# Kernel optimization log

Hardware: AMD Instinct MI355X
Metric: run time of the kernel (lower is better)

Reference implementation:

```python
import jax, jax.numpy as jnp
import numpy as np

B, M, FIN = 16, 49152, 16
F1, K = 32, 5
NNZ = 8 * M  # ~8 neighbors per vertex on a HEALPix sphere mesh


def setup_inputs() -> dict:
    key = jax.random.key(0)
    kx, kr, kc, kv, kw, kb = jax.random.split(key, 6)
    x = jax.random.normal(kx, (B, M, FIN), dtype=jnp.float32)
    rows = jax.random.randint(kr, (NNZ,), 0, M, dtype=jnp.int32)
    cols = jax.random.randint(kc, (NNZ,), 0, M, dtype=jnp.int32)
    # small values keep the order-K Chebyshev recurrence numerically tame
    vals = jax.random.normal(kv, (NNZ,), dtype=jnp.float32) * 0.1
    stddev = 1.0 / np.sqrt(FIN * (K + 0.5) / 2.0)
    kernel = jax.random.normal(kw, (FIN * K, F1), dtype=jnp.float32) * stddev
    bias = jax.random.uniform(kb, (1, 1, F1), dtype=jnp.float32) * 0.05
    return {"x": x, "rows": rows, "cols": cols, "vals": vals,
            "kernel": kernel, "bias": bias}


def reference(x, rows, cols, vals, kernel, bias):
    # x: [B, M, Fin]; sparse Laplacian L in COO (rows, cols, vals), shape [M, M]
    b, m, fin = x.shape
    k = kernel.shape[0] // fin

    def spmm(X):  # L @ X for X: [M, Fin*B]
        return jax.ops.segment_sum(vals[:, None] * X[cols], rows, num_segments=m)

    # x0: [M, Fin*B] exactly as the TF transpose/reshape does
    x0 = jnp.transpose(x, (1, 2, 0)).reshape(m, fin * b)
    xs = [x0]
    if k > 1:
        x1 = spmm(x0)
        xs.append(x1)
    for _ in range(2, k):
        x2 = 2.0 * spmm(x1) - x0
        xs.append(x2)
        x0, x1 = x1, x2
    # [K, M, Fin, B] -> [B, M, Fin, K] -> [B*M, Fin*K]
    xk = jnp.stack(xs, axis=0).reshape(k, m, fin, b)
    xk = jnp.transpose(xk, (3, 1, 2, 0)).reshape(b * m, fin * k)
    out = (xk @ kernel).reshape(b, m, -1)  # [B, M, F1]
    return out + bias
```

## Files before the change

### kernel.cpp

```cpp
#include <hip/hip_runtime.h>


constexpr int M   = 49152;
constexpr int B   = 16;
constexpr int FIN = 16;
constexpr int F1  = 32;
constexpr int K   = 5;
constexpr int XBS = M * FIN;
constexpr size_t SLICEB   = (size_t)M * 64;
constexpr size_t BUFBYTES = (size_t)M * 512;
constexpr int NBLK_M = M / 256;
constexpr int NHB = 64 * NBLK_M;

typedef short s16x8 __attribute__((ext_vector_type(8)));
typedef float f32x4 __attribute__((ext_vector_type(4)));
typedef unsigned int u32;
typedef unsigned long long u64;

#define DEVFN __device__ __forceinline__

DEVFN float lo2f(u32 d) {
  union { u32 u; float f; } v; v.u = d << 16; return v.f;
}
DEVFN float hi2f(u32 d) {
  union { u32 u; float f; } v; v.u = d & 0xffff0000u; return v.f;
}
DEVFN unsigned short f2bf(float f) {
  union { float f; u32 u; } v;
  v.f = f;
  u32 r = (v.u + 0x7FFFu + ((v.u >> 16) & 1u)) >> 16;
  return (unsigned short)r;
}


__global__ __launch_bounds__(256) void transform_x(const float* __restrict__ x,
                                                   char* __restrict__ x0b) {
  int lane = threadIdx.x & 63, wave = threadIdx.x >> 6;
  int mchunk = blockIdx.x >> 2, bquad = blockIdx.x & 3;
  int b = bquad * 4 + wave;
  int m = mchunk * 16 + (lane >> 2);
  int f = (lane & 3) * 4;
  float4 v = *(const float4*)(x + (size_t)b * XBS + (size_t)m * FIN + f);
  ushort4 r = make_ushort4(f2bf(v.x), f2bf(v.y), f2bf(v.z), f2bf(v.w));
  *(ushort4*)(x0b + (size_t)(b >> 1) * SLICEB + (size_t)m * 64 +
              (size_t)(b & 1) * 32 + (size_t)(lane & 3) * 8) = r;
}


__global__ __launch_bounds__(256) void hist_kernel(const int* __restrict__ rows,
                                                   int* __restrict__ counts, int nnz) {
  int i = blockIdx.x * 256 + threadIdx.x;
  if (i < nnz) atomicAdd(&counts[rows[i]], 1);
}

__global__ __launch_bounds__(256) void pad_counts(const int* __restrict__ counts,
                                                  int* __restrict__ c8) {
  int m = blockIdx.x * 256 + threadIdx.x;
  c8[m] = (counts[m] + 8) & ~7;
}

DEVFN int wave_incl_scan(int v, int lane) {
#pragma unroll
  for (int off = 1; off < 64; off <<= 1) {
    int t = __shfl_up(v, off);
    if (lane >= off) v += t;
  }
  return v;
}

__global__ __launch_bounds__(1024) void scan_blocks(const int* __restrict__ src,
                                                    int* __restrict__ dst,
                                                    int* __restrict__ partials) {
  __shared__ int wsum[16];
  int tid = threadIdx.x, lane = tid & 63, w = tid >> 6;
  int i = blockIdx.x * 1024 + tid;
  int s = wave_incl_scan(src[i], lane);
  if (lane == 63) wsum[w] = s;
  __syncthreads();
  if (tid < 16) {
    int t = wsum[tid];
#pragma unroll
    for (int off = 1; off < 16; off <<= 1) {
      int u = __shfl_up(t, off);
      if (tid >= off) t += u;
    }
    wsum[tid] = t;
  }
  __syncthreads();
  int base = (w > 0) ? wsum[w - 1] : 0;
  s += base;
  dst[i + 1] = s;
  if (tid == 1023) partials[blockIdx.x] = s;
}

__global__ void scan_partials_kernel(int* __restrict__ partials,
                                     int* __restrict__ dst, int nblk) {
  int lane = threadIdx.x;
  int v = (lane < nblk) ? partials[lane] : 0;
  v = wave_incl_scan(v, lane);
  if (lane < nblk) partials[lane] = v;
  if (lane == 0) dst[0] = 0;
}

__global__ __launch_bounds__(1024) void scan_add_kernel(int* __restrict__ dst,
                                                        const int* __restrict__ partials) {
  if (blockIdx.x == 0) return;
  int i = blockIdx.x * 1024 + threadIdx.x;
  dst[i + 1] += partials[blockIdx.x - 1];
}

__global__ __launch_bounds__(256) void scatter_kernel(const int* __restrict__ rows,
                                                      const int* __restrict__ cols,
                                                      const float* __restrict__ vals,
                                                      const int* __restrict__ row_ptr8,
                                                      int* __restrict__ fill,
                                                      u32* __restrict__ cvp, int nnz) {
  int i = blockIdx.x * 256 + threadIdx.x;
  if (i < nnz) {
    int r = rows[i];
    int pos = row_ptr8[r] + atomicAdd(&fill[r], 1);
    cvp[pos] = ((u32)cols[i] << 16) | (u32)f2bf(vals[i]);
  }
}


__global__ __launch_bounds__(256) void deg_hist_blk(const int* __restrict__ counts,
                                                    int* __restrict__ blkhist) {
  __shared__ int lh[64];
  int tid = threadIdx.x;
  if (tid < 64) lh[tid] = 0;
  __syncthreads();
  int m = blockIdx.x * 256 + tid;
  atomicAdd(&lh[min(counts[m], 63)], 1);
  __syncthreads();
  if (tid < 64) blkhist[tid * NBLK_M + blockIdx.x] = lh[tid];
}

__global__ __launch_bounds__(256) void perm_scatter_blk(const int* __restrict__ counts,
                                                        const int* __restrict__ sc,
                                                        int* __restrict__ perm) {
  __shared__ int lh[64];
  __shared__ int lbase[64];
  int tid = threadIdx.x, blk = blockIdx.x;
  if (tid < 64) lh[tid] = 0;
  __syncthreads();
  int m = blk * 256 + tid;
  int d = min(counts[m], 63);
  int lr = atomicAdd(&lh[d], 1);
  __syncthreads();
  if (tid < 64) lbase[tid] = sc[tid * NBLK_M + blk];
  __syncthreads();
  perm[lbase[d] + lr] = m;
}


template <bool SUB>
__global__ __launch_bounds__(256) void spmm_pad(const char* __restrict__ xsrc,
                                                const char* __restrict__ ssrc,
                                                char* __restrict__ y,
                                                const int* __restrict__ row_ptr8,
                                                const int* __restrict__ perm,
                                                const u32* __restrict__ cvp) {
  int s  = blockIdx.x & 7;
  int g4 = blockIdx.x >> 3;
  int lane = threadIdx.x & 63, wave = threadIdx.x >> 6;
  int r = lane >> 3, q = lane & 7;
  int grp = g4 * 4 + wave;
  const char* sbase = xsrc + (size_t)s * SLICEB;
  size_t qb = (size_t)q * 8;

  int ridA = perm[grp * 16 + r];
  int ridB = perm[grp * 16 + 8 + r];
  int baseA = row_ptr8[ridA], baseB = row_ptr8[ridB];
  int plimA = row_ptr8[ridA + 1] - baseA - 1;
  int plimB = row_ptr8[ridB + 1] - baseB - 1;

  int wns = (max(plimA, plimB) + 1) >> 3;
  wns = max(wns, __shfl_xor(wns, 8));
  wns = max(wns, __shfl_xor(wns, 16));
  wns = max(wns, __shfl_xor(wns, 32));

  u64 svA = 0, svB = 0;
  if (SUB) {
    svA = __builtin_nontemporal_load(
        (const u64*)(ssrc + (size_t)s * SLICEB + (size_t)ridA * 64 + qb));
    svB = __builtin_nontemporal_load(
        (const u64*)(ssrc + (size_t)s * SLICEB + (size_t)ridB * 64 + qb));
  }

  float aA0 = 0.f, aA1 = 0.f, aA2 = 0.f, aA3 = 0.f;
  float aB0 = 0.f, aB1 = 0.f, aB2 = 0.f, aB3 = 0.f;
  int nedge = wns * 8;
  for (int t0 = 0; t0 < nedge; t0 += 8) {
    u32 cA[8], cB[8];
    u64 dA[8], dB[8];
#pragma unroll
    for (int t = 0; t < 8; ++t) cA[t] = cvp[baseA + min(t0 + t, plimA)];
#pragma unroll
    for (int t = 0; t < 8; ++t) cB[t] = cvp[baseB + min(t0 + t, plimB)];
#pragma unroll
    for (int t = 0; t < 8; ++t)
      dA[t] = *(const u64*)(sbase + (size_t)(cA[t] >> 16) * 64 + qb);
#pragma unroll
    for (int t = 0; t < 8; ++t)
      dB[t] = *(const u64*)(sbase + (size_t)(cB[t] >> 16) * 64 + qb);
#pragma unroll
    for (int t = 0; t < 8; ++t) {
      float v = lo2f(cA[t]);
      u32 dl = (u32)dA[t], dh = (u32)(dA[t] >> 32);
      aA0 = fmaf(v, lo2f(dl), aA0); aA1 = fmaf(v, hi2f(dl), aA1);
      aA2 = fmaf(v, lo2f(dh), aA2); aA3 = fmaf(v, hi2f(dh), aA3);
    }
#pragma unroll
    for (int t = 0; t < 8; ++t) {
      float v = lo2f(cB[t]);
      u32 dl = (u32)dB[t], dh = (u32)(dB[t] >> 32);
      aB0 = fmaf(v, lo2f(dl), aB0); aB1 = fmaf(v, hi2f(dl), aB1);
      aB2 = fmaf(v, lo2f(dh), aB2); aB3 = fmaf(v, hi2f(dh), aB3);
    }
  }

  if (SUB) {
    u32 sl = (u32)svA, sh = (u32)(svA >> 32);
    aA0 = fmaf(2.f, aA0, -lo2f(sl)); aA1 = fmaf(2.f, aA1, -hi2f(sl));
    aA2 = fmaf(2.f, aA2, -lo2f(sh)); aA3 = fmaf(2.f, aA3, -hi2f(sh));
    sl = (u32)svB; sh = (u32)(svB >> 32);
    aB0 = fmaf(2.f, aB0, -lo2f(sl)); aB1 = fmaf(2.f, aB1, -hi2f(sl));
    aB2 = fmaf(2.f, aB2, -lo2f(sh)); aB3 = fmaf(2.f, aB3, -hi2f(sh));
  }
  u64 rvA = ((u64)(((u32)f2bf(aA3) << 16) | (u32)f2bf(aA2)) << 32) |
            (u64)(((u32)f2bf(aA1) << 16) | (u32)f2bf(aA0));
  u64 rvB = ((u64)(((u32)f2bf(aB3) << 16) | (u32)f2bf(aB2)) << 32) |
            (u64)(((u32)f2bf(aB1) << 16) | (u32)f2bf(aB0));
  __builtin_nontemporal_store(
      rvA, (u64*)(y + (size_t)s * SLICEB + (size_t)ridA * 64 + qb));
  __builtin_nontemporal_store(
      rvB, (u64*)(y + (size_t)s * SLICEB + (size_t)ridB * 64 + qb));
}


__global__ __launch_bounds__(256) void cheb_gemm_mfma(const char* __restrict__ xs0,
                                                      const float* __restrict__ kern,
                                                      const float* __restrict__ bias,
                                                      float* __restrict__ out) {
  __shared__ unsigned short bl[3][4][32][8];
  __shared__ float bsl[32];
  int tid = threadIdx.x;
  for (int idx = tid; idx < 3 * 4 * 32 * 8; idx += 256) {
    int j = idx & 7, o = (idx >> 3) & 31, g = (idx >> 8) & 3, c = idx >> 10;
    int k = 2 * c + (g >> 1), f = (g & 1) * 8 + j;
    bl[c][g][o][j] = (k < K) ? f2bf(kern[(f * K + k) * F1 + o]) : (unsigned short)0;
  }
  if (tid < 32) bsl[tid] = bias[tid];
  __syncthreads();

  int lane = tid & 63, wave = tid >> 6;
  int pair = blockIdx.x & 7;
  int bb = wave & 1;
  int mtg = (blockIdx.x >> 3) * 2 + (wave >> 1);
  int b = pair * 2 + bb;
  int mt0 = mtg * 8;

  int row = lane & 15, g = lane >> 4;
  int col = lane & 15;

  s16x8 bf[3][2];
#pragma unroll
  for (int c = 0; c < 3; ++c) {
#pragma unroll
    for (int ot = 0; ot < 2; ++ot)
      bf[c][ot] = *(const s16x8*)(&bl[c][g][col + 16 * ot][0]);
  }
  float bias0 = bsl[col], bias1 = bsl[col + 16];

  size_t lanebyte = (size_t)pair * SLICEB + (size_t)row * 64 +
                    (size_t)bb * 32 + (size_t)(g & 1) * 16;
  int khalf = g >> 1;
  const char* p0 = xs0 + (size_t)(0 + khalf) * BUFBYTES + lanebyte;
  const char* p1 = xs0 + (size_t)(2 + khalf) * BUFBYTES + lanebyte;
  const char* p2 = xs0 + (size_t)(4 + khalf) * BUFBYTES + lanebyte;

  size_t obase0 = ((size_t)b * M + (size_t)mt0 * 16) * F1;

#pragma unroll 2
  for (int t = 0; t < 8; ++t) {
    size_t moff = (size_t)(mt0 + t) * (16 * 64);
    s16x8 a0 = *(const s16x8*)(p0 + moff);
    s16x8 a1 = *(const s16x8*)(p1 + moff);
    s16x8 a2 = (g < 2) ? *(const s16x8*)(p2 + moff) : (s16x8)0;

    f32x4 acc0 = {0.f, 0.f, 0.f, 0.f};
    f32x4 acc1 = {0.f, 0.f, 0.f, 0.f};
    acc0 = __builtin_amdgcn_mfma_f32_16x16x32_bf16(a0, bf[0][0], acc0, 0, 0, 0);
    acc1 = __builtin_amdgcn_mfma_f32_16x16x32_bf16(a0, bf[0][1], acc1, 0, 0, 0);
    acc0 = __builtin_amdgcn_mfma_f32_16x16x32_bf16(a1, bf[1][0], acc0, 0, 0, 0);
    acc1 = __builtin_amdgcn_mfma_f32_16x16x32_bf16(a1, bf[1][1], acc1, 0, 0, 0);
    acc0 = __builtin_amdgcn_mfma_f32_16x16x32_bf16(a2, bf[2][0], acc0, 0, 0, 0);
    acc1 = __builtin_amdgcn_mfma_f32_16x16x32_bf16(a2, bf[2][1], acc1, 0, 0, 0);

    float* ob = out + obase0 + (size_t)t * (16 * F1);
#pragma unroll
    for (int j = 0; j < 4; ++j) {
      int r = g * 4 + j;
      ob[r * F1 + col]      = acc0[j] + bias0;
      ob[r * F1 + col + 16] = acc1[j] + bias1;
    }
  }
}


extern "C" void kernel_launch(void* const* d_in, const int* in_sizes, int n_in,
                              void* d_out, int out_size, void* d_ws, size_t ws_size,
                              hipStream_t stream) {
  const float* x    = (const float*)d_in[0];
  const int*   rows = (const int*)d_in[1];
  const int*   cols = (const int*)d_in[2];
  const float* vals = (const float*)d_in[3];
  const float* kern = (const float*)d_in[4];
  const float* bias = (const float*)d_in[5];
  float* out = (float*)d_out;
  int nnz = in_sizes[1];
  int padWords = nnz + 8 * M + 256;

  char* x0b = (char*)d_ws;
  char* x1b = x0b + BUFBYTES;
  char* x2b = x1b + BUFBYTES;
  char* x3b = x2b + BUFBYTES;
  char* x4b = x3b + BUFBYTES;
  int* row_ptr8 = (int*)(x4b + BUFBYTES);
  int* counts   = row_ptr8 + (M + 256);
  int* fill     = counts + M;
  int* c8       = fill + M;
  int* partials = c8 + M;
  int* blkhist  = partials + 256;
  int* sc       = blkhist + NHB;
  int* perm     = sc + NHB + 256;
  u32* cvp8     = (u32*)(perm + M);

  int nblk1024 = M / 1024;
  int nblkH    = NHB / 1024;
  int nblkNnz  = (nnz + 255) / 256;

  transform_x<<<(M / 16) * 4, 256, 0, stream>>>(x, x0b);

  hipMemsetAsync(counts, 0, (size_t)2 * M * 4, stream);
  hipMemsetAsync(cvp8, 0, (size_t)padWords * 4, stream);
  hist_kernel<<<nblkNnz, 256, 0, stream>>>(rows, counts, nnz);
  pad_counts<<<NBLK_M, 256, 0, stream>>>(counts, c8);
  scan_blocks<<<nblk1024, 1024, 0, stream>>>(c8, row_ptr8, partials);
  scan_partials_kernel<<<1, 64, 0, stream>>>(partials, row_ptr8, nblk1024);
  scan_add_kernel<<<nblk1024, 1024, 0, stream>>>(row_ptr8, partials);
  deg_hist_blk<<<NBLK_M, 256, 0, stream>>>(counts, blkhist);
  scan_blocks<<<nblkH, 1024, 0, stream>>>(blkhist, sc, partials);
  scan_partials_kernel<<<1, 64, 0, stream>>>(partials, sc, nblkH);
  scan_add_kernel<<<nblkH, 1024, 0, stream>>>(sc, partials);
  perm_scatter_blk<<<NBLK_M, 256, 0, stream>>>(counts, sc, perm);
  scatter_kernel<<<nblkNnz, 256, 0, stream>>>(rows, cols, vals, row_ptr8, fill, cvp8, nnz);

  int spmmGrid = 8 * (M / 64);
  spmm_pad<false><<<spmmGrid, 256, 0, stream>>>(x0b, nullptr, x1b, row_ptr8, perm, cvp8);
  spmm_pad<true ><<<spmmGrid, 256, 0, stream>>>(x1b, x0b, x2b, row_ptr8, perm, cvp8);
  spmm_pad<true ><<<spmmGrid, 256, 0, stream>>>(x2b, x1b, x3b, row_ptr8, perm, cvp8);
  spmm_pad<true ><<<spmmGrid, 256, 0, stream>>>(x3b, x2b, x4b, row_ptr8, perm, cvp8);

  cheb_gemm_mfma<<<1536, 256, 0, stream>>>(x0b, kern, bias, out);

  (void)n_in; (void)out_size; (void)ws_size; (void)in_sizes;
}
```

Measured before the change: 303.8 us.

## Widen SpMM gathers to 16-byte lanes, fuse pad into degree histogram, vectorize GEMM stores

The SpMM kernel now assigns 16 rows per wave with 4 lanes per row, each lane gathering 16 bytes per neighbor instead of 8, which halves the number of gather instructions and per-lane column-index loads. The pad_counts kernel is folded into deg_hist_blk, so one launch disappears. The GEMM's B-fragment column mapping is permuted so each lane writes adjacent output columns as a single float2 store. The trade-offs are that each wave now handles a single 16-row group, not two interleaved 8-row sets, and each lane keeps 16-byte gather registers, which may reduce latency hiding.

```diff
diff --git a/kernel.cpp b/kernel.cpp
--- a/kernel.cpp
+++ b/kernel.cpp
@@ -16,6 +16,7 @@
 typedef float f32x4 __attribute__((ext_vector_type(4)));
 typedef unsigned int u32;
 typedef unsigned long long u64;
+typedef u32 u32x4 __attribute__((ext_vector_type(4)));
 
 #define DEVFN __device__ __forceinline__
 
@@ -53,12 +54,6 @@
   if (i < nnz) atomicAdd(&counts[rows[i]], 1);
 }
 
-__global__ __launch_bounds__(256) void pad_counts(const int* __restrict__ counts,
-                                                  int* __restrict__ c8) {
-  int m = blockIdx.x * 256 + threadIdx.x;
-  c8[m] = (counts[m] + 8) & ~7;
-}
-
 DEVFN int wave_incl_scan(int v, int lane) {
 #pragma unroll
   for (int off = 1; off < 64; off <<= 1) {
@@ -125,13 +120,16 @@
 
 
 __global__ __launch_bounds__(256) void deg_hist_blk(const int* __restrict__ counts,
+                                                    int* __restrict__ c8,
                                                     int* __restrict__ blkhist) {
   __shared__ int lh[64];
   int tid = threadIdx.x;
   if (tid < 64) lh[tid] = 0;
   __syncthreads();
   int m = blockIdx.x * 256 + tid;
-  atomicAdd(&lh[min(counts[m], 63)], 1);
+  int d = counts[m];
+  c8[m] = (d + 8) & ~7;
+  atomicAdd(&lh[min(d, 63)], 1);
   __syncthreads();
   if (tid < 64) blkhist[tid * NBLK_M + blockIdx.x] = lh[tid];
 }
@@ -155,87 +153,73 @@
 
 
 template <bool SUB>
-__global__ __launch_bounds__(256) void spmm_pad(const char* __restrict__ xsrc,
-                                                const char* __restrict__ ssrc,
-                                                char* __restrict__ y,
-                                                const int* __restrict__ row_ptr8,
-                                                const int* __restrict__ perm,
-                                                const u32* __restrict__ cvp) {
+__global__ __launch_bounds__(256) void spmm_pad16(const char* __restrict__ xsrc,
+                                                  const char* __restrict__ ssrc,
+                                                  char* __restrict__ y,
+                                                  const int* __restrict__ row_ptr8,
+                                                  const int* __restrict__ perm,
+                                                  const u32* __restrict__ cvp) {
   int s  = blockIdx.x & 7;
   int g4 = blockIdx.x >> 3;
   int lane = threadIdx.x & 63, wave = threadIdx.x >> 6;
-  int r = lane >> 3, q = lane & 7;
+  int r = lane >> 2, q2 = lane & 3;
   int grp = g4 * 4 + wave;
   const char* sbase = xsrc + (size_t)s * SLICEB;
-  size_t qb = (size_t)q * 8;
-
-  int ridA = perm[grp * 16 + r];
-  int ridB = perm[grp * 16 + 8 + r];
-  int baseA = row_ptr8[ridA], baseB = row_ptr8[ridB];
-  int plimA = row_ptr8[ridA + 1] - baseA - 1;
-  int plimB = row_ptr8[ridB + 1] - baseB - 1;
-
-  int wns = (max(plimA, plimB) + 1) >> 3;
+  size_t qb = (size_t)q2 * 16;
+
+  int rid  = perm[grp * 16 + r];
+  int base = row_ptr8[rid];
+  int plim = row_ptr8[rid + 1] - base - 1;
+
+  int wns = (plim + 1) >> 3;
+  wns = max(wns, __shfl_xor(wns, 4));
   wns = max(wns, __shfl_xor(wns, 8));
   wns = max(wns, __shfl_xor(wns, 16));
   wns = max(wns, __shfl_xor(wns, 32));
 
-  u64 svA = 0, svB = 0;
+  u64 sv0 = 0, sv1 = 0;
   if (SUB) {
-    svA = __builtin_nontemporal_load(
-        (const u64*)(ssrc + (size_t)s * SLICEB + (size_t)ridA * 64 + qb));
-    svB = __builtin_nontemporal_load(
-        (const u64*)(ssrc + (size_t)s * SLICEB + (size_t)ridB * 64 + qb));
-  }
-
-  float aA0 = 0.f, aA1 = 0.f, aA2 = 0.f, aA3 = 0.f;
-  float aB0 = 0.f, aB1 = 0.f, aB2 = 0.f, aB3 = 0.f;
+    const char* sp = ssrc + (size_t)s * SLICEB + (size_t)rid * 64 + qb;
+    sv0 = __builtin_nontemporal_load((const u64*)sp);
+    sv1 = __builtin_nontemporal_load((const u64*)(sp + 8));
+  }
+
+  float a0 = 0.f, a1 = 0.f, a2 = 0.f, a3 = 0.f;
+  float a4 = 0.f, a5 = 0.f, a6 = 0.f, a7 = 0.f;
   int nedge = wns * 8;
   for (int t0 = 0; t0 < nedge; t0 += 8) {
-    u32 cA[8], cB[8];
-    u64 dA[8], dB[8];
-#pragma unroll
-    for (int t = 0; t < 8; ++t) cA[t] = cvp[baseA + min(t0 + t, plimA)];
-#pragma unroll
-    for (int t = 0; t < 8; ++t) cB[t] = cvp[baseB + min(t0 + t, plimB)];
+    u32 cA[8];
+    u32x4 dA[8];
+#pragma unroll
+    for (int t = 0; t < 8; ++t) cA[t] = cvp[base + min(t0 + t, plim)];
 #pragma unroll
     for (int t = 0; t < 8; ++t)
-      dA[t] = *(const u64*)(sbase + (size_t)(cA[t] >> 16) * 64 + qb);
-#pragma unroll
-    for (int t = 0; t < 8; ++t)
-      dB[t] = *(const u64*)(sbase + (size_t)(cB[t] >> 16) * 64 + qb);
+      dA[t] = *(const u32x4*)(sbase + (size_t)(cA[t] >> 16) * 64 + qb);
 #pragma unroll
     for (int t = 0; t < 8; ++t) {
       float v = lo2f(cA[t]);
-      u32 dl = (u32)dA[t], dh = (u32)(dA[t] >> 32);
-      aA0 = fmaf(v, lo2f(dl), aA0); aA1 = fmaf(v, hi2f(dl), aA1);
-      aA2 = fmaf(v, lo2f(dh), aA2); aA3 = fmaf(v, hi2f(dh), aA3);
+      a0 = fmaf(v, lo2f(dA[t].x), a0); a1 = fmaf(v, hi2f(dA[t].x), a1);
+      a2 = fmaf(v, lo2f(dA[t].y), a2); a3 = fmaf(v, hi2f(dA[t].y), a3);
+      a4 = fmaf(v, lo2f(dA[t].z), a4); a5 = fmaf(v, hi2f(dA[t].z), a5);
+      a6 = fmaf(v, lo2f(dA[t].w), a6); a7 = fmaf(v, hi2f(dA[t].w), a7);
     }
-#pragma unroll
-    for (int t = 0; t < 8; ++t) {
-      float v = lo2f(cB[t]);
-      u32 dl = (u32)dB[t], dh = (u32)(dB[t] >> 32);
-      aB0 = fmaf(v, lo2f(dl), aB0); aB1 = fmaf(v, hi2f(dl), aB1);
-      aB2 = fmaf(v, lo2f(dh), aB2); aB3 = fmaf(v, hi2f(dh), aB3);
-    }
   }
 
   if (SUB) {
-    u32 sl = (u32)svA, sh = (u32)(svA >> 32);
-    aA0 = fmaf(2.f, aA0, -lo2f(sl)); aA1 = fmaf(2.f, aA1, -hi2f(sl));
-    aA2 = fmaf(2.f, aA2, -lo2f(sh)); aA3 = fmaf(2.f, aA3, -hi2f(sh));
-    sl = (u32)svB; sh = (u32)(svB >> 32);
-    aB0 = fmaf(2.f, aB0, -lo2f(sl)); aB1 = fmaf(2.f, aB1, -hi2f(sl));
-    aB2 = fmaf(2.f, aB2, -lo2f(sh)); aB3 = fmaf(2.f, aB3, -hi2f(sh));
-  }
-  u64 rvA = ((u64)(((u32)f2bf(aA3) << 16) | (u32)f2bf(aA2)) << 32) |
-            (u64)(((u32)f2bf(aA1) << 16) | (u32)f2bf(aA0));
-  u64 rvB = ((u64)(((u32)f2bf(aB3) << 16) | (u32)f2bf(aB2)) << 32) |
-            (u64)(((u32)f2bf(aB1) << 16) | (u32)f2bf(aB0));
-  __builtin_nontemporal_store(
-      rvA, (u64*)(y + (size_t)s * SLICEB + (size_t)ridA * 64 + qb));
-  __builtin_nontemporal_store(
-      rvB, (u64*)(y + (size_t)s * SLICEB + (size_t)ridB * 64 + qb));
+    u32 s0 = (u32)sv0, s1 = (u32)(sv0 >> 32);
+    u32 s2 = (u32)sv1, s3 = (u32)(sv1 >> 32);
+    a0 = fmaf(2.f, a0, -lo2f(s0)); a1 = fmaf(2.f, a1, -hi2f(s0));
+    a2 = fmaf(2.f, a2, -lo2f(s1)); a3 = fmaf(2.f, a3, -hi2f(s1));
+    a4 = fmaf(2.f, a4, -lo2f(s2)); a5 = fmaf(2.f, a5, -hi2f(s2));
+    a6 = fmaf(2.f, a6, -lo2f(s3)); a7 = fmaf(2.f, a7, -hi2f(s3));
+  }
+  u64 rv0 = ((u64)(((u32)f2bf(a3) << 16) | (u32)f2bf(a2)) << 32) |
+            (u64)(((u32)f2bf(a1) << 16) | (u32)f2bf(a0));
+  u64 rv1 = ((u64)(((u32)f2bf(a7) << 16) | (u32)f2bf(a6)) << 32) |
+            (u64)(((u32)f2bf(a5) << 16) | (u32)f2bf(a4));
+  char* yp = y + (size_t)s * SLICEB + (size_t)rid * 64 + qb;
+  __builtin_nontemporal_store(rv0, (u64*)yp);
+  __builtin_nontemporal_store(rv1, (u64*)(yp + 8));
 }
 
 
@@ -269,9 +253,9 @@
   for (int c = 0; c < 3; ++c) {
 #pragma unroll
     for (int ot = 0; ot < 2; ++ot)
-      bf[c][ot] = *(const s16x8*)(&bl[c][g][col + 16 * ot][0]);
-  }
-  float bias0 = bsl[col], bias1 = bsl[col + 16];
+      bf[c][ot] = *(const s16x8*)(&bl[c][g][2 * col + ot][0]);
+  }
+  float bias0 = bsl[2 * col], bias1 = bsl[2 * col + 1];
 
   size_t lanebyte = (size_t)pair * SLICEB + (size_t)row * 64 +
                     (size_t)bb * 32 + (size_t)(g & 1) * 16;
@@ -302,8 +286,8 @@
 #pragma unroll
     for (int j = 0; j < 4; ++j) {
       int r = g * 4 + j;
-      ob[r * F1 + col]      = acc0[j] + bias0;
-      ob[r * F1 + col + 16] = acc1[j] + bias1;
+      float2 st = make_float2(acc0[j] + bias0, acc1[j] + bias1);
+      *(float2*)(ob + r * F1 + 2 * col) = st;
     }
   }
 }
@@ -346,11 +330,10 @@
   hipMemsetAsync(counts, 0, (size_t)2 * M * 4, stream);
   hipMemsetAsync(cvp8, 0, (size_t)padWords * 4, stream);
   hist_kernel<<<nblkNnz, 256, 0, stream>>>(rows, counts, nnz);
-  pad_counts<<<NBLK_M, 256, 0, stream>>>(counts, c8);
+  deg_hist_blk<<<NBLK_M, 256, 0, stream>>>(counts, c8, blkhist);
   scan_blocks<<<nblk1024, 1024, 0, stream>>>(c8, row_ptr8, partials);
   scan_partials_kernel<<<1, 64, 0, stream>>>(partials, row_ptr8, nblk1024);
   scan_add_kernel<<<nblk1024, 1024, 0, stream>>>(row_ptr8, partials);
-  deg_hist_blk<<<NBLK_M, 256, 0, stream>>>(counts, blkhist);
   scan_blocks<<<nblkH, 1024, 0, stream>>>(blkhist, sc, partials);
   scan_partials_kernel<<<1, 64, 0, stream>>>(partials, sc, nblkH);
   scan_add_kernel<<<nblkH, 1024, 0, stream>>>(sc, partials);
@@ -358,10 +341,10 @@
   scatter_kernel<<<nblkNnz, 256, 0, stream>>>(rows, cols, vals, row_ptr8, fill, cvp8, nnz);
 
   int spmmGrid = 8 * (M / 64);
-  spmm_pad<false><<<spmmGrid, 256, 0, stream>>>(x0b, nullptr, x1b, row_ptr8, perm, cvp8);
-  spmm_pad<true ><<<spmmGrid, 256, 0, stream>>>(x1b, x0b, x2b, row_ptr8, perm, cvp8);
-  spmm_pad<true ><<<spmmGrid, 256, 0, stream>>>(x2b, x1b, x3b, row_ptr8, perm, cvp8);
-  spmm_pad<true ><<<spmmGrid, 256, 0, stream>>>(x3b, x2b, x4b, row_ptr8, perm, cvp8);
+  spmm_pad16<false><<<spmmGrid, 256, 0, stream>>>(x0b, nullptr, x1b, row_ptr8, perm, cvp8);
+  spmm_pad16<true ><<<spmmGrid, 256, 0, stream>>>(x1b, x0b, x2b, row_ptr8, perm, cvp8);
+  spmm_pad16<true ><<<spmmGrid, 256, 0, stream>>>(x2b, x1b, x3b, row_ptr8, perm, cvp8);
+  spmm_pad16<true ><<<spmmGrid, 256, 0, stream>>>(x3b, x2b, x4b, row_ptr8, perm, cvp8);
 
   cheb_gemm_mfma<<<1536, 256, 0, stream>>>(x0b, kern, bias, out);
 
```

Measured after the change: 282.9 us. 6.9% less time.
